# Kernel optimization log

Hardware: AMD Instinct MI355X
Metric: run time of the kernel (lower is better)

The kernel has to match this reference:

```python
import jax, jax.numpy as jnp
import numpy as np

B = 16          # number of trees (batch)
H = 256         # hidden_size == feature_size
S = 16          # Tree.num_sem
C = 5           # max_child_num (complete C-ary tree)
L = 6           # tree depth: leaves at level L, internal levels 0..L-1
N_LEAF = C**L                     # 15625
N_INT = (C**L - 1) // (C - 1)     # 3906 internal nodes, level-l offset = (C^l-1)/(C-1)


def setup_inputs() -> dict:
    key = jax.random.key(0)
    ks = jax.random.split(key, 20)
    rn = lambda k, shp, s=0.05: jax.random.normal(k, shp, dtype=jnp.float32) * s
    return {
        "leaf_box": jax.random.normal(ks[0], (B, N_LEAF, 4), dtype=jnp.float32),
        "leaf_sem": jax.random.uniform(ks[1], (B, N_LEAF, S), dtype=jnp.float32),
        "internal_box": jax.random.normal(ks[2], (B, N_INT, 4), dtype=jnp.float32),
        "node_type": jax.random.randint(ks[3], (B, N_INT), 0, 3, dtype=jnp.int32),
        "eps": jax.random.normal(ks[4], (B, H), dtype=jnp.float32),
        "W_box": rn(ks[5], (4, H)), "b_box": jnp.zeros((H,), jnp.float32),
        "W_sem": rn(ks[6], (S, H)), "b_sem": jnp.zeros((H,), jnp.float32),
        "W_node": rn(ks[7], (3, C * H, H)), "b_node": jnp.zeros((3, H), jnp.float32),
        "W1": rn(ks[8], (H, H)), "b1": jnp.zeros((H,), jnp.float32),
        "Wmu": rn(ks[9], (H, H)), "bmu": jnp.zeros((H,), jnp.float32),
        "Wvar": rn(ks[10], (H, H)), "bvar": jnp.zeros((H,), jnp.float32),
    }


def reference(leaf_box, leaf_sem, internal_box, node_type, eps,
              W_box, b_box, W_sem, b_sem, W_node, b_node,
              W1, b1, Wmu, bmu, Wvar, bvar):
    box_enc = lambda b: jax.nn.relu(b @ W_box + b_box)
    # LeafEncoder: relu-box-encoding + relu-sem-encoding
    feats = box_enc(leaf_box) + jax.nn.relu(leaf_sem @ W_sem + b_sem)  # [B, N_LEAF, H]
    # Bottom-up over internal levels (static loop over L=6 levels)
    for l in range(L - 1, -1, -1):
        n = C ** l
        off = (C ** l - 1) // (C - 1)
        child = feats.reshape(B, n, C * H)  # children flattened per parent (child_exists==1)
        # Apply all 3 branch encoders (vertical/horizontal/stack), select by node label
        y_all = jnp.einsum('bnk,tkh->bnth', child, W_node) + b_node          # [B,n,3,H]
        sel = jax.nn.one_hot(node_type[:, off:off + n], 3, dtype=child.dtype)  # [B,n,3]
        y = jnp.einsum('bnth,bnt->bnh', y_all, sel)
        feats = jax.nn.relu(y) + box_enc(internal_box[:, off:off + n])
    root = feats[:, 0]  # [B, H]
    # Sampler (variational, probabilistic)
    enc = jax.nn.relu(root @ W1 + b1)
    mu = enc @ Wmu + bmu
    logvar = enc @ Wvar + bvar
    std = jnp.exp(0.5 * logvar)
    kld = 1.0 + logvar - mu ** 2 - jnp.exp(logvar)
    return jnp.concatenate([eps * std + mu, kld], axis=1)  # [B, 2H]
```

## Files before the change

### kernel.cpp

```cpp
#include <hip/hip_runtime.h>


#define B_ 16
#define H_ 256
#define NLEAF 15625
#define NINT 3906

typedef __bf16 bf16_t;
typedef bf16_t bf16x8 __attribute__((ext_vector_type(8)));
typedef bf16_t bf16x4 __attribute__((ext_vector_type(4)));
typedef float f32x4 __attribute__((ext_vector_type(4)));

__device__ __forceinline__ void gl2lds16(const bf16_t* g, bf16_t* l) {
  __builtin_amdgcn_global_load_lds((const __attribute__((address_space(1))) void*)g,
                                   (__attribute__((address_space(3))) void*)l,
                                   16, 0, 0);
}

__global__ __launch_bounds__(256) void prep_kernel(const float* __restrict__ W_node,
                                                   bf16_t* __restrict__ Wt,
                                                   int* __restrict__ counters) {
  if (blockIdx.x == 0 && threadIdx.x < 18) counters[threadIdx.x] = 0;
  const int t = blockIdx.x / 80;
  const int kc = blockIdx.x % 80;
  const int h = threadIdx.x;
  const float* srcp = W_node + (size_t)t * 1280 * 256 + h;
  bf16_t* dstp = Wt + ((size_t)(t * 256 + h)) * 1280;
#pragma unroll
  for (int k0 = kc * 16; k0 < kc * 16 + 16; k0 += 8) {
    bf16x8 v;
#pragma unroll
    for (int j = 0; j < 8; ++j) v[j] = (bf16_t)srcp[(size_t)(k0 + j) * 256];
    *(bf16x8*)(dstp + k0) = v;
  }
}

__global__ __launch_bounds__(256) void leaf_kernel(
    const float* __restrict__ leaf_box, const float* __restrict__ leaf_sem,
    const float* __restrict__ W_box, const float* __restrict__ b_box,
    const float* __restrict__ W_sem, const float* __restrict__ b_sem,
    bf16_t* __restrict__ f6) {
  const int lane = threadIdx.x & 63;
  const int wave = threadIdx.x >> 6;
  const int h0 = lane * 4;
  float wb[4][4], ws[16][4], bb[4], bs[4];
#pragma unroll
  for (int j = 0; j < 4; ++j) {
    float4 v = *(const float4*)(W_box + j * H_ + h0);
    wb[j][0] = v.x; wb[j][1] = v.y; wb[j][2] = v.z; wb[j][3] = v.w;
  }
#pragma unroll
  for (int j = 0; j < 16; ++j) {
    float4 v = *(const float4*)(W_sem + j * H_ + h0);
    ws[j][0] = v.x; ws[j][1] = v.y; ws[j][2] = v.z; ws[j][3] = v.w;
  }
  {
    float4 v = *(const float4*)(b_box + h0);
    bb[0] = v.x; bb[1] = v.y; bb[2] = v.z; bb[3] = v.w;
    float4 u = *(const float4*)(b_sem + h0);
    bs[0] = u.x; bs[1] = u.y; bs[2] = u.z; bs[3] = u.w;
  }
  const int ROWS = B_ * NLEAF;
  const int stride = gridDim.x * 4;
  for (int row = blockIdx.x * 4 + wave; row < ROWS; row += stride) {
    float4 bx = *(const float4*)(leaf_box + (size_t)row * 4);
    const float4* sp = (const float4*)(leaf_sem + (size_t)row * 16);
    float4 sv0 = sp[0], sv1 = sp[1], sv2 = sp[2], sv3 = sp[3];
    bf16x4 o;
#pragma unroll
    for (int c = 0; c < 4; ++c) {
      float s1 = fmaf(wb[0][c], bx.x, fmaf(wb[1][c], bx.y,
                 fmaf(wb[2][c], bx.z, fmaf(wb[3][c], bx.w, bb[c]))));
      float s2 = bs[c];
      s2 = fmaf(ws[0][c], sv0.x, s2);  s2 = fmaf(ws[1][c], sv0.y, s2);
      s2 = fmaf(ws[2][c], sv0.z, s2);  s2 = fmaf(ws[3][c], sv0.w, s2);
      s2 = fmaf(ws[4][c], sv1.x, s2);  s2 = fmaf(ws[5][c], sv1.y, s2);
      s2 = fmaf(ws[6][c], sv1.z, s2);  s2 = fmaf(ws[7][c], sv1.w, s2);
      s2 = fmaf(ws[8][c], sv2.x, s2);  s2 = fmaf(ws[9][c], sv2.y, s2);
      s2 = fmaf(ws[10][c], sv2.z, s2); s2 = fmaf(ws[11][c], sv2.w, s2);
      s2 = fmaf(ws[12][c], sv3.x, s2); s2 = fmaf(ws[13][c], sv3.y, s2);
      s2 = fmaf(ws[14][c], sv3.z, s2); s2 = fmaf(ws[15][c], sv3.w, s2);
      o[c] = (bf16_t)(fmaxf(s1, 0.f) + fmaxf(s2, 0.f));
    }
    *(bf16x4*)(f6 + (size_t)row * H_ + h0) = o;
  }
}

__global__ __launch_bounds__(256) void bucket_kernel(const int* __restrict__ node_type,
                                                     int* __restrict__ counters,
                                                     int2* __restrict__ buckets) {
  __shared__ int lcnt[18];
  __shared__ int lbase[18];
  const int tid = threadIdx.x;
  if (tid < 18) lcnt[tid] = 0;
  __syncthreads();

  int idx = blockIdx.x * 256 + tid;
  bool active = idx < B_ * NINT;
  int t = 0, key = 0, mypos = 0;
  int2 e;
  int base = 0, nl_cap = 0;
  if (active) {
    int b = idx / NINT;
    int j = idx - b * NINT;
    int l, off;
    if (j >= 781)      { l = 5; off = 781; }
    else if (j >= 156) { l = 4; off = 156; }
    else if (j >= 31)  { l = 3; off = 31; }
    else if (j >= 6)   { l = 2; off = 6; }
    else if (j >= 1)   { l = 1; off = 1; }
    else               { l = 0; off = 0; }
    const int n_tab[6]    = {1, 5, 25, 125, 625, 3125};
    const int nn_tab[6]   = {5, 25, 125, 625, 3125, 15625};
    const int base_tab[6] = {0, 48, 288, 1488, 7488, 37488};
    int n_l = n_tab[l], nn = nn_tab[l];
    t = node_type[idx];
    int i = j - off;
    e.x = b * n_l + i;
    e.y = b * nn + 5 * i;
    base = base_tab[l];
    nl_cap = B_ * n_l;
    key = l * 3 + t;
    mypos = atomicAdd(&lcnt[key], 1);
  }
  __syncthreads();
  if (tid < 18) {
    int c = lcnt[tid];
    lbase[tid] = c ? atomicAdd(&counters[tid], c) : 0;
  }
  __syncthreads();
  if (active) {
    buckets[base + t * nl_cap + lbase[key] + mypos] = e;
  }
}

__global__ __launch_bounds__(256) void level_kernel(
    const bf16_t* __restrict__ src, bf16_t* __restrict__ dst,
    const int2* __restrict__ bucket, const int* __restrict__ counters,
    const bf16_t* __restrict__ Wt, const float* __restrict__ b_node,
    const float* __restrict__ ibox, const float* __restrict__ W_box,
    const float* __restrict__ b_box, int n_l, int off_l, int cap) {
  const int t = blockIdx.y;
  const int cnt = counters[t];
  const int tile0 = blockIdx.x * 128;
  if (tile0 >= cnt) return;
  const int nblk = blockIdx.z;
  const int2* rd = bucket + (size_t)t * cap;

  __shared__ __align__(16) bf16_t Asm[2][128][64];
  __shared__ __align__(16) bf16_t Bsm[2][128][64];

  const int tid = threadIdx.x;
  const int lane = tid & 63;
  const int wave = tid >> 6;
  const int wm = wave & 1, wn = wave >> 1;
  const int quad = lane >> 4;
  const int l15 = lane & 15;

  const int r8 = tid >> 3;
  const int sc = tid & 7;
  const bf16_t* wsrc = Wt + ((size_t)t * 256 + nblk * 128) * 1280;
  const bf16_t* aptr[4];
  const bf16_t* bptr[4];
#pragma unroll
  for (int i = 0; i < 4; ++i) {
    int r = i * 32 + r8;
    int gch = sc ^ ((r >> 1) & 7);
    int ai = tile0 + r;
    if (ai >= cnt) ai = cnt - 1;
    aptr[i] = src + (size_t)rd[ai].y * H_ + gch * 8;
    bptr[i] = wsrc + (size_t)r * 1280 + gch * 8;
  }

  f32x4 acc[4][4];
#pragma unroll
  for (int i = 0; i < 4; ++i)
#pragma unroll
    for (int j = 0; j < 4; ++j) acc[i][j] = (f32x4){0.f, 0.f, 0.f, 0.f};

  const int sw = (l15 >> 1) & 7;
  const int pc0 = ((0 * 4 + quad) ^ sw) * 8;
  const int pc1 = ((1 * 4 + quad) ^ sw) * 8;

#define STAGE(buf, ks)                                          \
  {                                                             \
    const int ko = (ks) * 64;                                   \
    bf16_t* la = &Asm[buf][0][0] + wave * 512;                  \
    bf16_t* lb = &Bsm[buf][0][0] + wave * 512;                  \
    _Pragma("unroll") for (int i = 0; i < 4; ++i)               \
        gl2lds16(aptr[i] + ko, la + i * 2048);                  \
    _Pragma("unroll") for (int i = 0; i < 4; ++i)               \
        gl2lds16(bptr[i] + ko, lb + i * 2048);                  \
  }

  STAGE(0, 0)
  for (int ks = 0; ks < 20; ++ks) {
    const int buf = ks & 1;
    __syncthreads();
    bf16x8 af0[4], af1[4], bf0[4], bf1[4];
#pragma unroll
    for (int am = 0; am < 4; ++am) {
      af0[am] = *(const bf16x8*)(&Asm[buf][wm * 64 + am * 16 + l15][pc0]);
      af1[am] = *(const bf16x8*)(&Asm[buf][wm * 64 + am * 16 + l15][pc1]);
    }
#pragma unroll
    for (int bn = 0; bn < 4; ++bn) {
      bf0[bn] = *(const bf16x8*)(&Bsm[buf][wn * 64 + bn * 16 + l15][pc0]);
      bf1[bn] = *(const bf16x8*)(&Bsm[buf][wn * 64 + bn * 16 + l15][pc1]);
    }
    if (ks + 1 < 20) STAGE(buf ^ 1, ks + 1)
#pragma unroll
    for (int am = 0; am < 4; ++am)
#pragma unroll
      for (int bn = 0; bn < 4; ++bn)
        acc[am][bn] = __builtin_amdgcn_mfma_f32_16x16x32_bf16(af0[am], bf0[bn], acc[am][bn], 0, 0, 0);
#pragma unroll
    for (int am = 0; am < 4; ++am)
#pragma unroll
      for (int bn = 0; bn < 4; ++bn)
        acc[am][bn] = __builtin_amdgcn_mfma_f32_16x16x32_bf16(af1[am], bf1[bn], acc[am][bn], 0, 0, 0);
  }
#undef STAGE

  float wbv[4][6];
#pragma unroll
  for (int bn = 0; bn < 4; ++bn) {
    int col = nblk * 128 + wn * 64 + bn * 16 + l15;
    wbv[bn][0] = W_box[col];
    wbv[bn][1] = W_box[H_ + col];
    wbv[bn][2] = W_box[2 * H_ + col];
    wbv[bn][3] = W_box[3 * H_ + col];
    wbv[bn][4] = b_box[col];
    wbv[bn][5] = b_node[t * H_ + col];
  }
#pragma unroll
  for (int am = 0; am < 4; ++am) {
    int orow[4]; float4 bxv[4]; bool valid[4];
#pragma unroll
    for (int r = 0; r < 4; ++r) {
      int gidx = tile0 + wm * 64 + am * 16 + quad * 4 + r;
      valid[r] = (gidx < cnt);
      int ic = valid[r] ? gidx : (cnt - 1);
      int orw = rd[ic].x;
      orow[r] = orw;
      int b = orw / n_l;
      int i = orw - b * n_l;
      bxv[r] = *(const float4*)(ibox + ((size_t)b * NINT + off_l + i) * 4);
    }
#pragma unroll
    for (int bn = 0; bn < 4; ++bn) {
      int col = nblk * 128 + wn * 64 + bn * 16 + l15;
#pragma unroll
      for (int r = 0; r < 4; ++r) {
        if (!valid[r]) continue;
        float y = fmaxf(acc[am][bn][r] + wbv[bn][5], 0.f);
        float be = fmaf(wbv[bn][0], bxv[r].x,
                   fmaf(wbv[bn][1], bxv[r].y,
                   fmaf(wbv[bn][2], bxv[r].z,
                   fmaf(wbv[bn][3], bxv[r].w, wbv[bn][4]))));
        be = fmaxf(be, 0.f);
        dst[(size_t)orow[r] * H_ + col] = (bf16_t)(y + be);
      }
    }
  }
}

__global__ __launch_bounds__(256) void head_kernel(
    const bf16_t* __restrict__ f0, const float* __restrict__ eps,
    const float* __restrict__ W1, const float* __restrict__ b1,
    const float* __restrict__ Wmu, const float* __restrict__ bmu,
    const float* __restrict__ Wvar, const float* __restrict__ bvar,
    float* __restrict__ out) {
  __shared__ float root[256];
  __shared__ float enc[256];
  int b = blockIdx.x, h = threadIdx.x;
  root[h] = (float)f0[b * H_ + h];
  __syncthreads();
  float a = b1[h];
  for (int k = 0; k < 256; ++k) a = fmaf(root[k], W1[k * H_ + h], a);
  enc[h] = fmaxf(a, 0.f);
  __syncthreads();
  float m = bmu[h], lv = bvar[h];
  for (int k = 0; k < 256; ++k) {
    float e = enc[k];
    m = fmaf(e, Wmu[k * H_ + h], m);
    lv = fmaf(e, Wvar[k * H_ + h], lv);
  }
  float stdv = expf(0.5f * lv);
  float kld = 1.f + lv - m * m - expf(lv);
  out[b * 512 + h] = eps[b * H_ + h] * stdv + m;
  out[b * 512 + 256 + h] = kld;
}

extern "C" void kernel_launch(void* const* d_in, const int* in_sizes, int n_in,
                              void* d_out, int out_size, void* d_ws, size_t ws_size,
                              hipStream_t stream) {
  const float* leaf_box     = (const float*)d_in[0];
  const float* leaf_sem     = (const float*)d_in[1];
  const float* internal_box = (const float*)d_in[2];
  const int*   node_type    = (const int*)d_in[3];
  const float* eps          = (const float*)d_in[4];
  const float* W_box        = (const float*)d_in[5];
  const float* b_box        = (const float*)d_in[6];
  const float* W_sem        = (const float*)d_in[7];
  const float* b_sem        = (const float*)d_in[8];
  const float* W_node       = (const float*)d_in[9];
  const float* b_node       = (const float*)d_in[10];
  const float* W1           = (const float*)d_in[11];
  const float* b1           = (const float*)d_in[12];
  const float* Wmu          = (const float*)d_in[13];
  const float* bmu          = (const float*)d_in[14];
  const float* Wvar         = (const float*)d_in[15];
  const float* bvar         = (const float*)d_in[16];
  float* out = (float*)d_out;

  char* p = (char*)d_ws;
  auto alloc = [&](size_t bytes) {
    char* r = p;
    p += (bytes + 255) & ~(size_t)255;
    return r;
  };
  bf16_t* Wt = (bf16_t*)alloc((size_t)3 * 256 * 1280 * 2);
  const int n_tab[7] = {1, 5, 25, 125, 625, 3125, 15625};
  bf16_t* f[7];
  for (int l = 0; l <= 6; ++l) f[l] = (bf16_t*)alloc((size_t)B_ * n_tab[l] * H_ * 2);
  int* counters = (int*)alloc(18 * 4);
  int2* buckets = (int2*)alloc((size_t)187488 * 8);

  hipLaunchKernelGGL(prep_kernel, dim3(240), dim3(256), 0, stream, W_node, Wt, counters);
  hipLaunchKernelGGL(leaf_kernel, dim3(2048), dim3(256), 0, stream,
                     leaf_box, leaf_sem, W_box, b_box, W_sem, b_sem, f[6]);
  hipLaunchKernelGGL(bucket_kernel, dim3((B_ * NINT + 255) / 256), dim3(256), 0, stream,
                     node_type, counters, buckets);

  const int lvl_base[6] = {0, 48, 288, 1488, 7488, 37488};
  const int off_tab[6]  = {0, 1, 6, 31, 156, 781};
  for (int l = 5; l >= 0; --l) {
    int cap = B_ * n_tab[l];
    int tiles = (cap + 127) / 128;
    hipLaunchKernelGGL(level_kernel, dim3(tiles, 3, 2), dim3(256), 0, stream,
                       f[l + 1], f[l], buckets + lvl_base[l], counters + l * 3,
                       Wt, b_node, internal_box, W_box, b_box,
                       n_tab[l], off_tab[l], cap);
  }
  hipLaunchKernelGGL(head_kernel, dim3(16), dim3(256), 0, stream,
                     f[0], eps, W1, b1, Wmu, bmu, Wvar, bvar, out);
}
```

Baseline: 392.7 us.

## Load weight fragments directly from global, process two leaf rows per wave

The level GEMM kernel stops staging the weight tile through LDS and has each lane load its B-operand MFMA fragments straight from global memory, halving shared memory use and the LDS traffic. The leaf encoder now handles two rows per wave iteration to raise instruction-level parallelism, and the head kernel's dot-product loops are unrolled by eight. The direct global B loads are not double-buffered and are issued right after the barrier, so their latency may stall the MFMA loop. Weight rows are also read repeatedly across waves rather than shared through LDS.

Measured after the change: 507.9 us. +29.3%, slower.

```diff
diff --git a/kernel.cpp b/kernel.cpp
--- a/kernel.cpp
+++ b/kernel.cpp
@@ -61,28 +61,38 @@
     bs[0] = u.x; bs[1] = u.y; bs[2] = u.z; bs[3] = u.w;
   }
   const int ROWS = B_ * NLEAF;
-  const int stride = gridDim.x * 4;
-  for (int row = blockIdx.x * 4 + wave; row < ROWS; row += stride) {
-    float4 bx = *(const float4*)(leaf_box + (size_t)row * 4);
-    const float4* sp = (const float4*)(leaf_sem + (size_t)row * 16);
-    float4 sv0 = sp[0], sv1 = sp[1], sv2 = sp[2], sv3 = sp[3];
-    bf16x4 o;
+  const int stride = gridDim.x * 8;
+  for (int row = blockIdx.x * 8 + wave * 2; row < ROWS; row += stride) {
+    float4 bxA = *(const float4*)(leaf_box + (size_t)row * 4);
+    float4 bxB = *(const float4*)(leaf_box + (size_t)(row + 1) * 4);
+    const float4* spA = (const float4*)(leaf_sem + (size_t)row * 16);
+    const float4* spB = (const float4*)(leaf_sem + (size_t)(row + 1) * 16);
+    float4 svA[4] = {spA[0], spA[1], spA[2], spA[3]};
+    float4 svB[4] = {spB[0], spB[1], spB[2], spB[3]};
+    bf16x4 oA, oB;
 #pragma unroll
     for (int c = 0; c < 4; ++c) {
-      float s1 = fmaf(wb[0][c], bx.x, fmaf(wb[1][c], bx.y,
-                 fmaf(wb[2][c], bx.z, fmaf(wb[3][c], bx.w, bb[c]))));
-      float s2 = bs[c];
-      s2 = fmaf(ws[0][c], sv0.x, s2);  s2 = fmaf(ws[1][c], sv0.y, s2);
-      s2 = fmaf(ws[2][c], sv0.z, s2);  s2 = fmaf(ws[3][c], sv0.w, s2);
-      s2 = fmaf(ws[4][c], sv1.x, s2);  s2 = fmaf(ws[5][c], sv1.y, s2);
-      s2 = fmaf(ws[6][c], sv1.z, s2);  s2 = fmaf(ws[7][c], sv1.w, s2);
-      s2 = fmaf(ws[8][c], sv2.x, s2);  s2 = fmaf(ws[9][c], sv2.y, s2);
-      s2 = fmaf(ws[10][c], sv2.z, s2); s2 = fmaf(ws[11][c], sv2.w, s2);
-      s2 = fmaf(ws[12][c], sv3.x, s2); s2 = fmaf(ws[13][c], sv3.y, s2);
-      s2 = fmaf(ws[14][c], sv3.z, s2); s2 = fmaf(ws[15][c], sv3.w, s2);
-      o[c] = (bf16_t)(fmaxf(s1, 0.f) + fmaxf(s2, 0.f));
-    }
-    *(bf16x4*)(f6 + (size_t)row * H_ + h0) = o;
+      float s1A = fmaf(wb[0][c], bxA.x, fmaf(wb[1][c], bxA.y,
+                  fmaf(wb[2][c], bxA.z, fmaf(wb[3][c], bxA.w, bb[c]))));
+      float s1B = fmaf(wb[0][c], bxB.x, fmaf(wb[1][c], bxB.y,
+                  fmaf(wb[2][c], bxB.z, fmaf(wb[3][c], bxB.w, bb[c]))));
+      float s2A = bs[c], s2B = bs[c];
+#pragma unroll
+      for (int j = 0; j < 4; ++j) {
+        s2A = fmaf(ws[4*j+0][c], svA[j].x, s2A);
+        s2A = fmaf(ws[4*j+1][c], svA[j].y, s2A);
+        s2A = fmaf(ws[4*j+2][c], svA[j].z, s2A);
+        s2A = fmaf(ws[4*j+3][c], svA[j].w, s2A);
+        s2B = fmaf(ws[4*j+0][c], svB[j].x, s2B);
+        s2B = fmaf(ws[4*j+1][c], svB[j].y, s2B);
+        s2B = fmaf(ws[4*j+2][c], svB[j].z, s2B);
+        s2B = fmaf(ws[4*j+3][c], svB[j].w, s2B);
+      }
+      oA[c] = (bf16_t)(fmaxf(s1A, 0.f) + fmaxf(s2A, 0.f));
+      oB[c] = (bf16_t)(fmaxf(s1B, 0.f) + fmaxf(s2B, 0.f));
+    }
+    *(bf16x4*)(f6 + (size_t)row * H_ + h0) = oA;
+    *(bf16x4*)(f6 + (size_t)(row + 1) * H_ + h0) = oB;
   }
 }
 
@@ -148,7 +158,6 @@
   const int2* rd = bucket + (size_t)t * cap;
 
   __shared__ __align__(16) bf16_t Asm[2][128][64];
-  __shared__ __align__(16) bf16_t Bsm[2][128][64];
 
   const int tid = threadIdx.x;
   const int lane = tid & 63;
@@ -159,9 +168,7 @@
 
   const int r8 = tid >> 3;
   const int sc = tid & 7;
-  const bf16_t* wsrc = Wt + ((size_t)t * 256 + nblk * 128) * 1280;
   const bf16_t* aptr[4];
-  const bf16_t* bptr[4];
 #pragma unroll
   for (int i = 0; i < 4; ++i) {
     int r = i * 32 + r8;
@@ -169,7 +176,13 @@
     int ai = tile0 + r;
     if (ai >= cnt) ai = cnt - 1;
     aptr[i] = src + (size_t)rd[ai].y * H_ + gch * 8;
-    bptr[i] = wsrc + (size_t)r * 1280 + gch * 8;
+  }
+
+  const bf16_t* b_base[4];
+#pragma unroll
+  for (int bn = 0; bn < 4; ++bn) {
+    int col = nblk * 128 + wn * 64 + bn * 16 + l15;
+    b_base[bn] = Wt + ((size_t)t * 256 + col) * 1280 + quad * 8;
   }
 
   f32x4 acc[4][4];
@@ -182,45 +195,43 @@
   const int pc0 = ((0 * 4 + quad) ^ sw) * 8;
   const int pc1 = ((1 * 4 + quad) ^ sw) * 8;
 
-#define STAGE(buf, ks)                                          \
+#define STAGEA(buf, ks)                                         \
   {                                                             \
     const int ko = (ks) * 64;                                   \
     bf16_t* la = &Asm[buf][0][0] + wave * 512;                  \
-    bf16_t* lb = &Bsm[buf][0][0] + wave * 512;                  \
     _Pragma("unroll") for (int i = 0; i < 4; ++i)               \
         gl2lds16(aptr[i] + ko, la + i * 2048);                  \
-    _Pragma("unroll") for (int i = 0; i < 4; ++i)               \
-        gl2lds16(bptr[i] + ko, lb + i * 2048);                  \
-  }
-
-  STAGE(0, 0)
+  }
+
+  STAGEA(0, 0)
   for (int ks = 0; ks < 20; ++ks) {
     const int buf = ks & 1;
     __syncthreads();
-    bf16x8 af0[4], af1[4], bf0[4], bf1[4];
+    bf16x8 bg0[4], bg1[4];
+#pragma unroll
+    for (int bn = 0; bn < 4; ++bn) {
+      bg0[bn] = *(const bf16x8*)(b_base[bn] + ks * 64);
+      bg1[bn] = *(const bf16x8*)(b_base[bn] + ks * 64 + 32);
+    }
+    bf16x8 af0[4], af1[4];
 #pragma unroll
     for (int am = 0; am < 4; ++am) {
       af0[am] = *(const bf16x8*)(&Asm[buf][wm * 64 + am * 16 + l15][pc0]);
       af1[am] = *(const bf16x8*)(&Asm[buf][wm * 64 + am * 16 + l15][pc1]);
     }
-#pragma unroll
-    for (int bn = 0; bn < 4; ++bn) {
-      bf0[bn] = *(const bf16x8*)(&Bsm[buf][wn * 64 + bn * 16 + l15][pc0]);
-      bf1[bn] = *(const bf16x8*)(&Bsm[buf][wn * 64 + bn * 16 + l15][pc1]);
-    }
-    if (ks + 1 < 20) STAGE(buf ^ 1, ks + 1)
+    if (ks + 1 < 20) STAGEA(buf ^ 1, ks + 1)
 #pragma unroll
     for (int am = 0; am < 4; ++am)
 #pragma unroll
       for (int bn = 0; bn < 4; ++bn)
-        acc[am][bn] = __builtin_amdgcn_mfma_f32_16x16x32_bf16(af0[am], bf0[bn], acc[am][bn], 0, 0, 0);
+        acc[am][bn] = __builtin_amdgcn_mfma_f32_16x16x32_bf16(af0[am], bg0[bn], acc[am][bn], 0, 0, 0);
 #pragma unroll
     for (int am = 0; am < 4; ++am)
 #pragma unroll
       for (int bn = 0; bn < 4; ++bn)
-        acc[am][bn] = __builtin_amdgcn_mfma_f32_16x16x32_bf16(af1[am], bf1[bn], acc[am][bn], 0, 0, 0);
-  }
-#undef STAGE
+        acc[am][bn] = __builtin_amdgcn_mfma_f32_16x16x32_bf16(af1[am], bg1[bn], acc[am][bn], 0, 0, 0);
+  }
+#undef STAGEA
 
   float wbv[4][6];
 #pragma unroll
@@ -277,10 +288,12 @@
   root[h] = (float)f0[b * H_ + h];
   __syncthreads();
   float a = b1[h];
+#pragma unroll 8
   for (int k = 0; k < 256; ++k) a = fmaf(root[k], W1[k * H_ + h], a);
   enc[h] = fmaxf(a, 0.f);
   __syncthreads();
   float m = bmu[h], lv = bvar[h];
+#pragma unroll 8
   for (int k = 0; k < 256; ++k) {
     float e = enc[k];
     m = fmaf(e, Wmu[k * H_ + h], m);
```
